# Optimization experiments

Hardware: AMD Instinct MI355X
Metric: run time of the kernel (lower is better)

Reference implementation:

```python
import jax, jax.numpy as jnp
import numpy as np

IN_F = 512
OUT_F = 512
LMAX = 4
M = (LMAX + 1) ** 2  # 25
BATCH = 4096


def _expand_index():
    # l repeated (2l+1) times: [0, 1,1,1, 2,2,2,2,2, ...]
    return np.concatenate([np.full(2 * l + 1, l, dtype=np.int32) for l in range(LMAX + 1)])


def setup_inputs() -> dict:
    key = jax.random.key(0)
    k1, k2 = jax.random.split(key)
    bound = 1.0 / np.sqrt(IN_F)
    x = jax.random.normal(k1, (BATCH, IN_F * M, 1), dtype=jnp.float32)
    weight = jax.random.uniform(k2, (LMAX + 1, OUT_F, IN_F), dtype=jnp.float32,
                                minval=-bound, maxval=bound)
    bias = jnp.zeros((OUT_F,), dtype=jnp.float32)
    return {"input": x, "weight": weight, "bias": bias}


def reference(input, weight, bias):
    B = input.shape[0]
    idx = jnp.asarray(_expand_index())
    # gather-expand shared per-l weight to per-m weight: [M, out, in]
    w = weight[idx]
    # 'b (i m) n -> b m (i n)' with n=1  => [B, M, in]
    xi = input[..., 0].reshape(B, IN_F, M).transpose(0, 2, 1)
    # batched per-m linear: [B, M, out]
    out = jnp.einsum('bmi,moi->bmo', xi, w)
    # bias added only to the m=0 (l=0 scalar) component
    out = out.at[:, 0, :].add(bias)
    # 'b (m n) o -> b (o m) n' with n=1 => [B, out*M, 1]
    return out.transpose(0, 2, 1).reshape(B, OUT_F * M, 1)
```

## Files before the change

kernel.cpp:

```cpp
#include <hip/hip_runtime.h>
#include <hip/hip_bf16.h>


typedef __bf16 bf16x8v __attribute__((ext_vector_type(8)));
typedef float floatx4 __attribute__((ext_vector_type(4)));
typedef unsigned short ushort_t;
typedef unsigned short ushortx4 __attribute__((ext_vector_type(4)));

#define ROW_F 12800
#define PITCH 44
#define LDS_USH (400 * 44)

__device__ __forceinline__ ushort_t f2bf(float f) {
    __hip_bfloat16 h = __float2bfloat16(f);
    return __builtin_bit_cast(ushort_t, h);
}

__global__ void cvt_w_kernel(const float* __restrict__ w, ushort_t* __restrict__ wb) {
    int i = (blockIdx.x * 256 + threadIdx.x) * 4;
    floatx4 v = *reinterpret_cast<const floatx4*>(w + i);
    ushortx4 h;
    h.x = f2bf(v[0]); h.y = f2bf(v[1]); h.z = f2bf(v[2]); h.w = f2bf(v[3]);
    *reinterpret_cast<ushortx4*>(wb + i) = h;
}

__global__ __launch_bounds__(256, 2) void irrep_kernel(
        const float* __restrict__ x, const ushort_t* __restrict__ wb,
        const float* __restrict__ bias, float* __restrict__ out) {
    __shared__ __align__(16) ushort_t Asm[LDS_USH];

    const int tid = threadIdx.x, lane = tid & 63;
    const int wv = tid >> 6;
    const int lr = lane & 15, lh = lane >> 4;

    const int bid   = blockIdx.x;
    const int osib  = (bid >> 3) & 7;
    const int btile = (bid & 7) | ((bid >> 6) << 3);
    const int b0 = btile * 16, o0 = osib * 64, ow = o0 + wv * 16;

    constexpr int LOF[25] = {0,1,1,1,2,2,2,2,2,3,3,3,3,3,3,3,4,4,4,4,4,4,4,4,4};

    const float* gp[13]; int woff[13];
#pragma unroll
    for (int i = 0; i < 13; ++i) {
        int Q = tid + 256 * i;
        if (Q < 3200) {
            int bb = Q / 200, r = Q - bb * 200;
            int kq = r / 25, m = r - kq * 25;
            gp[i]  = x + (size_t)(b0 + bb) * ROW_F + kq * 100 + m;
            woff[i] = (bb * 25 + m) * PITCH + kq * 4;
        } else { gp[i] = x; woff[i] = 0; }
    }

    float vbuf[13][4];
    auto issue = [&]() {
#pragma unroll
        for (int i = 0; i < 13; ++i) if (tid + 256 * i < 3200) {
#pragma unroll
            for (int j = 0; j < 4; ++j) vbuf[i][j] = gp[i][j * 25];
            gp[i] += 800;
        }
    };
    auto scat = [&]() {
#pragma unroll
        for (int i = 0; i < 13; ++i) if (tid + 256 * i < 3200) {
            ushortx4 h;
#pragma unroll
            for (int j = 0; j < 4; ++j) h[j] = f2bf(vbuf[i][j]);
            *reinterpret_cast<ushortx4*>(&Asm[woff[i]]) = h;
        }
    };

    floatx4 acc[25];
#pragma unroll
    for (int m = 0; m < 25; ++m) acc[m] = (floatx4){0.f, 0.f, 0.f, 0.f};

    issue();
#pragma unroll 1
    for (int s = 0; s < 16; ++s) {
        __syncthreads();
        scat();
        __syncthreads();
        if (s < 15) issue();

        bf16x8v bfr[5];
#pragma unroll
        for (int l = 0; l < 5; ++l)
            bfr[l] = *reinterpret_cast<const bf16x8v*>(
                wb + (size_t)(l * 512 + ow + lr) * 512 + s * 32 + lh * 8);
#pragma unroll
        for (int m = 0; m < 25; ++m) {
            const bf16x8v a = *reinterpret_cast<const bf16x8v*>(
                &Asm[(lr * 25 + m) * PITCH + lh * 8]);
            acc[m] = __builtin_amdgcn_mfma_f32_16x16x32_bf16(a, bfr[LOF[m]], acc[m], 0, 0, 0);
        }
    }

    {
        float bv = bias[ow + lr];
#pragma unroll
        for (int r = 0; r < 4; ++r) acc[0][r] += bv;
    }

    float* ep = reinterpret_cast<float*>(Asm);
    constexpr int EPROW = 1608;
#pragma unroll 1
    for (int p = 0; p < 4; ++p) {
        __syncthreads();
        if (lh == p) {
#pragma unroll
            for (int m = 0; m < 25; ++m) {
                int cb = (wv * 16 + lr) * 25 + m;
#pragma unroll
                for (int r = 0; r < 4; ++r) ep[r * EPROW + cb] = acc[m][r];
            }
        }
        __syncthreads();
#pragma unroll 1
        for (int idx = tid; idx < 1600; idx += 256) {
            int rr = idx / 400, c4 = idx - rr * 400;
            floatx4 v = *reinterpret_cast<const floatx4*>(ep + rr * EPROW + c4 * 4);
            *reinterpret_cast<floatx4*>(
                out + (size_t)(b0 + p * 4 + rr) * ROW_F + o0 * 25 + c4 * 4) = v;
        }
    }
}

extern "C" void kernel_launch(void* const* d_in, const int* in_sizes, int n_in,
                              void* d_out, int out_size, void* d_ws, size_t ws_size,
                              hipStream_t stream) {
    const float* x    = (const float*)d_in[0];
    const float* w    = (const float*)d_in[1];
    const float* bias = (const float*)d_in[2];
    float* outp       = (float*)d_out;
    ushort_t* wb      = (ushort_t*)d_ws;

    cvt_w_kernel<<<1280, 256, 0, stream>>>(w, wb);
    irrep_kernel<<<2048, 256, 0, stream>>>(x, wb, bias, outp);
}
```

Before: 289.0 us.

## Use contiguous float4 global loads for input staging with scattered bf16 LDS writes

Replaces the four strided scalar global loads per thread with one contiguous 16-byte vector load from each input row, then scatters the four converted bf16 values individually into the LDS tile with wraparound index math. The LDS pitch changes from 44 to 46 to alter the bank mapping, and the occupancy hint in the launch bounds is dropped. This is meant to cut global memory transactions for the dominant input read. In exchange it adds 2-byte LDS stores and index arithmetic, and the compiler may now use more registers.

Result: slower. 406.7 us (+40.7%).

```diff
diff --git a/kernel.cpp b/kernel.cpp
--- a/kernel.cpp
+++ b/kernel.cpp
@@ -8,8 +8,8 @@
 typedef unsigned short ushortx4 __attribute__((ext_vector_type(4)));
 
 #define ROW_F 12800
-#define PITCH 44
-#define LDS_USH (400 * 44)
+#define PITCH 46
+#define LDS_USH (400 * 46)
 
 __device__ __forceinline__ ushort_t f2bf(float f) {
     __hip_bfloat16 h = __float2bfloat16(f);
@@ -24,7 +24,7 @@
     *reinterpret_cast<ushortx4*>(wb + i) = h;
 }
 
-__global__ __launch_bounds__(256, 2) void irrep_kernel(
+__global__ __launch_bounds__(256) void irrep_kernel(
         const float* __restrict__ x, const ushort_t* __restrict__ wb,
         const float* __restrict__ bias, float* __restrict__ out) {
     __shared__ __align__(16) ushort_t Asm[LDS_USH];
@@ -40,34 +40,37 @@
 
     constexpr int LOF[25] = {0,1,1,1,2,2,2,2,2,3,3,3,3,3,3,3,4,4,4,4,4,4,4,4,4};
 
-    const float* gp[13]; int woff[13];
+    int goffB[13], w0[13], m0a[13];
 #pragma unroll
-    for (int i = 0; i < 13; ++i) {
-        int Q = tid + 256 * i;
+    for (int it = 0; it < 13; ++it) {
+        int Q = tid + 256 * it;
         if (Q < 3200) {
-            int bb = Q / 200, r = Q - bb * 200;
-            int kq = r / 25, m = r - kq * 25;
-            gp[i]  = x + (size_t)(b0 + bb) * ROW_F + kq * 100 + m;
-            woff[i] = (bb * 25 + m) * PITCH + kq * 4;
-        } else { gp[i] = x; woff[i] = 0; }
+            int bb = Q / 200, q = Q - bb * 200;
+            int e0 = 4 * q;
+            int k0 = e0 / 25, m0 = e0 - k0 * 25;
+            goffB[it] = bb * 51200 + q * 16;
+            w0[it]    = (bb * 25 + m0) * PITCH + k0;
+            m0a[it]   = m0;
+        } else { goffB[it] = 0; w0[it] = 0; m0a[it] = 30; }
     }
 
-    float vbuf[13][4];
-    auto issue = [&]() {
+    floatx4 vbuf[13];
+    const char* xb = (const char*)x + (size_t)b0 * 51200;
+    auto issue = [&](int s) {
+        const char* base = xb + s * 3200;
 #pragma unroll
-        for (int i = 0; i < 13; ++i) if (tid + 256 * i < 3200) {
-#pragma unroll
-            for (int j = 0; j < 4; ++j) vbuf[i][j] = gp[i][j * 25];
-            gp[i] += 800;
-        }
+        for (int it = 0; it < 13; ++it) if (tid + 256 * it < 3200)
+            vbuf[it] = *reinterpret_cast<const floatx4*>(base + goffB[it]);
     };
     auto scat = [&]() {
 #pragma unroll
-        for (int i = 0; i < 13; ++i) if (tid + 256 * i < 3200) {
-            ushortx4 h;
+        for (int it = 0; it < 13; ++it) if (tid + 256 * it < 3200) {
 #pragma unroll
-            for (int j = 0; j < 4; ++j) h[j] = f2bf(vbuf[i][j]);
-            *reinterpret_cast<ushortx4*>(&Asm[woff[i]]) = h;
+            for (int u = 0; u < 4; ++u) {
+                int a = w0[it] + u * PITCH;
+                if (m0a[it] + u >= 25) a -= (25 * PITCH - 1);
+                Asm[a] = f2bf(vbuf[it][u]);
+            }
         }
     };
 
@@ -75,13 +78,13 @@
 #pragma unroll
     for (int m = 0; m < 25; ++m) acc[m] = (floatx4){0.f, 0.f, 0.f, 0.f};
 
-    issue();
+    issue(0);
 #pragma unroll 1
     for (int s = 0; s < 16; ++s) {
         __syncthreads();
         scat();
         __syncthreads();
-        if (s < 15) issue();
+        if (s < 15) issue(s + 1);
 
         bf16x8v bfr[5];
 #pragma unroll
```

## Widen block to 128 outputs with 8 waves splitting m across two halves

Applied to the files above, without the earlier changes.

Each block now covers 128 output features instead of 64 and runs 8 waves, with two wave groups splitting the 25 m-components (13/12) and each wave handling 32 outputs. The staged x tile in LDS now feeds twice as many output columns, halving the number of times each x tile is loaded and converted from global memory. Grid size drops to 1024 blocks, and the per-thread staging load falls from 13 to 7 slots. The split is uneven (13 vs 12 m-components, 4 vs 2 weight levels), which leaves the waves with unequal work. The larger LDS footprint may also reduce occupancy.

Measured after the change: 325.1 us. 1.12x slower.

```diff
diff --git a/kernel.cpp b/kernel.cpp
--- a/kernel.cpp
+++ b/kernel.cpp
@@ -9,7 +9,7 @@
 
 #define ROW_F 12800
 #define PITCH 44
-#define LDS_USH (400 * 44)
+#define SMEM_BYTES 51392
 
 __device__ __forceinline__ ushort_t f2bf(float f) {
     __hip_bfloat16 h = __float2bfloat16(f);
@@ -24,46 +24,50 @@
     *reinterpret_cast<ushortx4*>(wb + i) = h;
 }
 
-__global__ __launch_bounds__(256, 2) void irrep_kernel(
+__global__ __launch_bounds__(512, 2) void irrep_kernel(
         const float* __restrict__ x, const ushort_t* __restrict__ wb,
         const float* __restrict__ bias, float* __restrict__ out) {
-    __shared__ __align__(16) ushort_t Asm[LDS_USH];
+    __shared__ __align__(16) unsigned char smem[SMEM_BYTES];
+    ushort_t* Asm = reinterpret_cast<ushort_t*>(smem);
 
     const int tid = threadIdx.x, lane = tid & 63;
     const int wv = tid >> 6;
     const int lr = lane & 15, lh = lane >> 4;
+    const int mh = wv >> 2;
+    const int oq = wv & 3;
 
     const int bid   = blockIdx.x;
-    const int osib  = (bid >> 3) & 7;
-    const int btile = (bid & 7) | ((bid >> 6) << 3);
-    const int b0 = btile * 16, o0 = osib * 64, ow = o0 + wv * 16;
+    const int osib  = (bid >> 3) & 3;
+    const int btile = (bid & 7) | ((bid >> 5) << 3);
+    const int b0 = btile * 16, o0 = osib * 128;
+    const int ob = o0 + oq * 32;
 
-    constexpr int LOF[25] = {0,1,1,1,2,2,2,2,2,3,3,3,3,3,3,3,4,4,4,4,4,4,4,4,4};
-
-    const float* gp[13]; int woff[13];
+    int goff[7], woff[7];
 #pragma unroll
-    for (int i = 0; i < 13; ++i) {
-        int Q = tid + 256 * i;
+    for (int i = 0; i < 7; ++i) {
+        int Q = tid + 512 * i;
         if (Q < 3200) {
             int bb = Q / 200, r = Q - bb * 200;
             int kq = r / 25, m = r - kq * 25;
-            gp[i]  = x + (size_t)(b0 + bb) * ROW_F + kq * 100 + m;
+            goff[i] = bb * ROW_F + kq * 100 + m;
             woff[i] = (bb * 25 + m) * PITCH + kq * 4;
-        } else { gp[i] = x; woff[i] = 0; }
+        } else { goff[i] = 0; woff[i] = 0; }
     }
+    const float* xb = x + (size_t)b0 * ROW_F;
 
-    float vbuf[13][4];
+    float vbuf[7][4];
     auto issue = [&]() {
 #pragma unroll
-        for (int i = 0; i < 13; ++i) if (tid + 256 * i < 3200) {
+        for (int i = 0; i < 7; ++i) if (tid + 512 * i < 3200) {
+            const float* p = xb + goff[i];
 #pragma unroll
-            for (int j = 0; j < 4; ++j) vbuf[i][j] = gp[i][j * 25];
-            gp[i] += 800;
+            for (int j = 0; j < 4; ++j) vbuf[i][j] = p[j * 25];
+            goff[i] += 800;
         }
     };
     auto scat = [&]() {
 #pragma unroll
-        for (int i = 0; i < 13; ++i) if (tid + 256 * i < 3200) {
+        for (int i = 0; i < 7; ++i) if (tid + 512 * i < 3200) {
             ushortx4 h;
 #pragma unroll
             for (int j = 0; j < 4; ++j) h[j] = f2bf(vbuf[i][j]);
@@ -71,9 +75,11 @@
         }
     };
 
-    floatx4 acc[25];
+    floatx4 acc[13][2];
 #pragma unroll
-    for (int m = 0; m < 25; ++m) acc[m] = (floatx4){0.f, 0.f, 0.f, 0.f};
+    for (int mm = 0; mm < 13; ++mm)
+#pragma unroll
+        for (int of = 0; of < 2; ++of) acc[mm][of] = (floatx4){0.f, 0.f, 0.f, 0.f};
 
     issue();
 #pragma unroll 1
@@ -83,42 +89,82 @@
         __syncthreads();
         if (s < 15) issue();
 
-        bf16x8v bfr[5];
+        if (mh == 0) {
+            bf16x8v bfr[4][2];
 #pragma unroll
-        for (int l = 0; l < 5; ++l)
-            bfr[l] = *reinterpret_cast<const bf16x8v*>(
-                wb + (size_t)(l * 512 + ow + lr) * 512 + s * 32 + lh * 8);
+            for (int l = 0; l < 4; ++l)
 #pragma unroll
-        for (int m = 0; m < 25; ++m) {
-            const bf16x8v a = *reinterpret_cast<const bf16x8v*>(
-                &Asm[(lr * 25 + m) * PITCH + lh * 8]);
-            acc[m] = __builtin_amdgcn_mfma_f32_16x16x32_bf16(a, bfr[LOF[m]], acc[m], 0, 0, 0);
+                for (int of = 0; of < 2; ++of)
+                    bfr[l][of] = *reinterpret_cast<const bf16x8v*>(
+                        wb + (size_t)(l * 512 + ob + of * 16 + lr) * 512 + s * 32 + lh * 8);
+            constexpr int L0[13] = {0,1,1,1,2,2,2,2,2,3,3,3,3};
+#pragma unroll
+            for (int mm = 0; mm < 13; ++mm) {
+                const bf16x8v a = *reinterpret_cast<const bf16x8v*>(
+                    &Asm[(lr * 25 + mm) * PITCH + lh * 8]);
+                acc[mm][0] = __builtin_amdgcn_mfma_f32_16x16x32_bf16(a, bfr[L0[mm]][0], acc[mm][0], 0, 0, 0);
+                acc[mm][1] = __builtin_amdgcn_mfma_f32_16x16x32_bf16(a, bfr[L0[mm]][1], acc[mm][1], 0, 0, 0);
+            }
+        } else {
+            bf16x8v bfr[2][2];
+#pragma unroll
+            for (int li = 0; li < 2; ++li)
+#pragma unroll
+                for (int of = 0; of < 2; ++of)
+                    bfr[li][of] = *reinterpret_cast<const bf16x8v*>(
+                        wb + (size_t)((li + 3) * 512 + ob + of * 16 + lr) * 512 + s * 32 + lh * 8);
+            constexpr int L1[12] = {0,0,0,1,1,1,1,1,1,1,1,1};
+#pragma unroll
+            for (int mm = 0; mm < 12; ++mm) {
+                const bf16x8v a = *reinterpret_cast<const bf16x8v*>(
+                    &Asm[(lr * 25 + 13 + mm) * PITCH + lh * 8]);
+                acc[mm][0] = __builtin_amdgcn_mfma_f32_16x16x32_bf16(a, bfr[L1[mm]][0], acc[mm][0], 0, 0, 0);
+                acc[mm][1] = __builtin_amdgcn_mfma_f32_16x16x32_bf16(a, bfr[L1[mm]][1], acc[mm][1], 0, 0, 0);
+            }
         }
     }
 
-    {
-        float bv = bias[ow + lr];
+    if (mh == 0) {
 #pragma unroll
-        for (int r = 0; r < 4; ++r) acc[0][r] += bv;
+        for (int of = 0; of < 2; ++of) {
+            float bv = bias[ob + of * 16 + lr];
+#pragma unroll
+            for (int r = 0; r < 4; ++r) acc[0][of][r] += bv;
+        }
     }
 
-    float* ep = reinterpret_cast<float*>(Asm);
-    constexpr int EPROW = 1608;
+    float* ep = reinterpret_cast<float*>(smem);
+    constexpr int EPROW = 3208;
 #pragma unroll 1
     for (int p = 0; p < 4; ++p) {
         __syncthreads();
         if (lh == p) {
+            if (mh == 0) {
 #pragma unroll
-            for (int m = 0; m < 25; ++m) {
-                int cb = (wv * 16 + lr) * 25 + m;
+                for (int of = 0; of < 2; ++of) {
+                    int cb = (oq * 32 + of * 16 + lr) * 25;
 #pragma unroll
-                for (int r = 0; r < 4; ++r) ep[r * EPROW + cb] = acc[m][r];
+                    for (int mm = 0; mm < 13; ++mm)
+#pragma unroll
+                        for (int r = 0; r < 4; ++r)
+                            ep[r * EPROW + cb + mm] = acc[mm][of][r];
+                }
+            } else {
+#pragma unroll
+                for (int of = 0; of < 2; ++of) {
+                    int cb = (oq * 32 + of * 16 + lr) * 25 + 13;
+#pragma unroll
+                    for (int mm = 0; mm < 12; ++mm)
+#pragma unroll
+                        for (int r = 0; r < 4; ++r)
+                            ep[r * EPROW + cb + mm] = acc[mm][of][r];
+                }
             }
         }
         __syncthreads();
 #pragma unroll 1
-        for (int idx = tid; idx < 1600; idx += 256) {
-            int rr = idx / 400, c4 = idx - rr * 400;
+        for (int idx = tid; idx < 3200; idx += 512) {
+            int rr = idx / 800, c4 = idx - rr * 800;
             floatx4 v = *reinterpret_cast<const floatx4*>(ep + rr * EPROW + c4 * 4);
             *reinterpret_cast<floatx4*>(
                 out + (size_t)(b0 + p * 4 + rr) * ROW_F + o0 * 25 + c4 * 4) = v;
@@ -136,5 +182,5 @@
     ushort_t* wb      = (ushort_t*)d_ws;
 
     cvt_w_kernel<<<1280, 256, 0, stream>>>(w, wb);
-    irrep_kernel<<<2048, 256, 0, stream>>>(x, wb, bias, outp);
+    irrep_kernel<<<1024, 512, 0, stream>>>(x, wb, bias, outp);
 }
```

## Split input transpose-to-bf16 into a separate pass, then direct-load GEMM

Applied to the files above, without the earlier changes.

Adds a pre-pass kernel that converts the input to bf16 and transposes it into a [B, M, in] layout in workspace. The GEMM kernel then loads A fragments straight from global memory, with no LDS staging or barriers in the main loop. The goal is to remove the strided gather, in-kernel conversion and syncthreads overhead from the fused kernel. In exchange it costs an extra full write and read of a 100 MB intermediate, and it needs a large workspace, otherwise the code falls back to the old kernel.

Result: slower. 542.5 us (+87.7%).

```diff
diff --git a/kernel.cpp b/kernel.cpp
--- a/kernel.cpp
+++ b/kernel.cpp
@@ -8,8 +8,8 @@
 typedef unsigned short ushortx4 __attribute__((ext_vector_type(4)));
 
 #define ROW_F 12800
+#define XT_BYTES 104857600ULL
 #define PITCH 44
-#define LDS_USH (400 * 44)
 
 __device__ __forceinline__ ushort_t f2bf(float f) {
     __hip_bfloat16 h = __float2bfloat16(f);
@@ -24,10 +24,33 @@
     *reinterpret_cast<ushortx4*>(wb + i) = h;
 }
 
-__global__ __launch_bounds__(256, 2) void irrep_kernel(
-        const float* __restrict__ x, const ushort_t* __restrict__ wb,
+__global__ __launch_bounds__(256) void xpose_kernel(
+        const float* __restrict__ x, ushort_t* __restrict__ xt) {
+    int gid = blockIdx.x * 256 + threadIdx.x;
+    int b = gid >> 7, ioq = gid & 127;
+
+    const floatx4* src = reinterpret_cast<const floatx4*>(x + (size_t)b * ROW_F + ioq * 100);
+    floatx4 f4[25];
+#pragma unroll
+    for (int j = 0; j < 25; ++j) f4[j] = src[j];
+
+    ushort_t* dst = xt + (size_t)b * 12800 + ioq * 4;
+#pragma unroll
+    for (int m = 0; m < 25; ++m) {
+        ushortx4 h;
+#pragma unroll
+        for (int d = 0; d < 4; ++d) {
+            int idx = d * 25 + m;
+            h[d] = f2bf(f4[idx >> 2][idx & 3]);
+        }
+        *reinterpret_cast<ushortx4*>(dst + (size_t)m * 512) = h;
+    }
+}
+
+__global__ __launch_bounds__(256) void gemm_kernel(
+        const ushort_t* __restrict__ xt, const ushort_t* __restrict__ wb,
         const float* __restrict__ bias, float* __restrict__ out) {
-    __shared__ __align__(16) ushort_t Asm[LDS_USH];
+    __shared__ __align__(16) float ep[4 * 1608];
 
     const int tid = threadIdx.x, lane = tid & 63;
     const int wv = tid >> 6;
@@ -40,6 +63,68 @@
 
     constexpr int LOF[25] = {0,1,1,1,2,2,2,2,2,3,3,3,3,3,3,3,4,4,4,4,4,4,4,4,4};
 
+    floatx4 acc[25];
+#pragma unroll
+    for (int m = 0; m < 25; ++m) acc[m] = (floatx4){0.f, 0.f, 0.f, 0.f};
+
+    const ushort_t* abase = xt + (size_t)(b0 + lr) * 12800 + lh * 8;
+    const ushort_t* bbase = wb + (size_t)(ow + lr) * 512 + lh * 8;
+
+#pragma unroll 1
+    for (int s = 0; s < 16; ++s) {
+        const ushort_t* ab = abase + s * 32;
+        const ushort_t* bb = bbase + s * 32;
+        bf16x8v bfr[5];
+#pragma unroll
+        for (int l = 0; l < 5; ++l)
+            bfr[l] = *reinterpret_cast<const bf16x8v*>(bb + (size_t)l * 262144);
+#pragma unroll
+        for (int m = 0; m < 25; ++m) {
+            const bf16x8v a = *reinterpret_cast<const bf16x8v*>(ab + (size_t)m * 512);
+            acc[m] = __builtin_amdgcn_mfma_f32_16x16x32_bf16(a, bfr[LOF[m]], acc[m], 0, 0, 0);
+        }
+    }
+
+    {
+        float bv = bias[ow + lr];
+#pragma unroll
+        for (int r = 0; r < 4; ++r) acc[0][r] += bv;
+    }
+
+    constexpr int EPROW = 1608;
+#pragma unroll 1
+    for (int p = 0; p < 4; ++p) {
+        __syncthreads();
+        if (lh == p) {
+#pragma unroll
+            for (int m = 0; m < 25; ++m) {
+                int cb = (wv * 16 + lr) * 25 + m;
+#pragma unroll
+                for (int r = 0; r < 4; ++r) ep[r * EPROW + cb] = acc[m][r];
+            }
+        }
+        __syncthreads();
+#pragma unroll 1
+        for (int idx = tid; idx < 1600; idx += 256) {
+            int rr = idx / 400, c4 = idx - rr * 400;
+            floatx4 v = *reinterpret_cast<const floatx4*>(ep + rr * EPROW + c4 * 4);
+            *reinterpret_cast<floatx4*>(
+                out + (size_t)(b0 + p * 4 + rr) * ROW_F + o0 * 25 + c4 * 4) = v;
+        }
+    }
+}
+
+__global__ __launch_bounds__(256, 2) void irrep_fb_kernel(
+        const float* __restrict__ x, const ushort_t* __restrict__ wb,
+        const float* __restrict__ bias, float* __restrict__ out) {
+    __shared__ __align__(16) ushort_t Asm[400 * PITCH];
+    const int tid = threadIdx.x, lane = tid & 63;
+    const int wv = tid >> 6, lr = lane & 15, lh = lane >> 4;
+    const int bid = blockIdx.x;
+    const int osib = (bid >> 3) & 7;
+    const int btile = (bid & 7) | ((bid >> 6) << 3);
+    const int b0 = btile * 16, o0 = osib * 64, ow = o0 + wv * 16;
+    constexpr int LOF[25] = {0,1,1,1,2,2,2,2,2,3,3,3,3,3,3,3,4,4,4,4,4,4,4,4,4};
     const float* gp[13]; int woff[13];
 #pragma unroll
     for (int i = 0; i < 13; ++i) {
@@ -47,11 +132,10 @@
         if (Q < 3200) {
             int bb = Q / 200, r = Q - bb * 200;
             int kq = r / 25, m = r - kq * 25;
-            gp[i]  = x + (size_t)(b0 + bb) * ROW_F + kq * 100 + m;
+            gp[i] = x + (size_t)(b0 + bb) * ROW_F + kq * 100 + m;
             woff[i] = (bb * 25 + m) * PITCH + kq * 4;
         } else { gp[i] = x; woff[i] = 0; }
     }
-
     float vbuf[13][4];
     auto issue = [&]() {
 #pragma unroll
@@ -70,11 +154,9 @@
             *reinterpret_cast<ushortx4*>(&Asm[woff[i]]) = h;
         }
     };
-
     floatx4 acc[25];
 #pragma unroll
     for (int m = 0; m < 25; ++m) acc[m] = (floatx4){0.f, 0.f, 0.f, 0.f};
-
     issue();
 #pragma unroll 1
     for (int s = 0; s < 16; ++s) {
@@ -82,7 +164,6 @@
         scat();
         __syncthreads();
         if (s < 15) issue();
-
         bf16x8v bfr[5];
 #pragma unroll
         for (int l = 0; l < 5; ++l)
@@ -95,13 +176,9 @@
             acc[m] = __builtin_amdgcn_mfma_f32_16x16x32_bf16(a, bfr[LOF[m]], acc[m], 0, 0, 0);
         }
     }
-
-    {
-        float bv = bias[ow + lr];
-#pragma unroll
-        for (int r = 0; r < 4; ++r) acc[0][r] += bv;
-    }
-
+    { float bv = bias[ow + lr];
+#pragma unroll
+      for (int r = 0; r < 4; ++r) acc[0][r] += bv; }
     float* ep = reinterpret_cast<float*>(Asm);
     constexpr int EPROW = 1608;
 #pragma unroll 1
@@ -133,8 +210,16 @@
     const float* w    = (const float*)d_in[1];
     const float* bias = (const float*)d_in[2];
     float* outp       = (float*)d_out;
-    ushort_t* wb      = (ushort_t*)d_ws;
-
-    cvt_w_kernel<<<1280, 256, 0, stream>>>(w, wb);
-    irrep_kernel<<<2048, 256, 0, stream>>>(x, wb, bias, outp);
-}
+
+    if (ws_size >= XT_BYTES + 2621440ULL + 256) {
+        ushort_t* xt = (ushort_t*)d_ws;
+        ushort_t* wbp = (ushort_t*)((char*)d_ws + XT_BYTES);
+        cvt_w_kernel<<<1280, 256, 0, stream>>>(w, wbp);
+        xpose_kernel<<<2048, 256, 0, stream>>>(x, xt);
+        gemm_kernel<<<2048, 256, 0, stream>>>(xt, wbp, bias, outp);
+    } else {
+        ushort_t* wbp = (ushort_t*)d_ws;
+        cvt_w_kernel<<<1280, 256, 0, stream>>>(w, wbp);
+        irrep_fb_kernel<<<2048, 256, 0, stream>>>(x, wbp, bias, outp);
+    }
+}
```
